# Optimization experiments

Hardware: AMD Instinct MI355X
Metric: run time of the kernel (lower is better)

Reference implementation:

```python
import jax, jax.numpy as jnp
import numpy as np

FP8_MAX = 448.0  # finfo(float8_e4m3fn).max
BLK = 128        # block_size = [128, 128]


def _quant_dequant_act(x):
    """Dynamic per-token, per-128-block fp8 quantization followed by dequant.
    Matches fp8_act_quant: scale = amax(block)/448, q = fp8(x/scale), deq = q*scale."""
    T, K = x.shape
    xb = x.reshape(T, K // BLK, BLK)
    amax = jnp.max(jnp.abs(xb), axis=-1, keepdims=True)
    scale = jnp.maximum(amax, 1e-12) / FP8_MAX  # [T, K//BLK, 1]
    q = (xb / scale).astype(jnp.float8_e4m3fn).astype(jnp.float32)
    return (q * scale).reshape(T, K)


def _dequant_weight(w, s):
    """Block-wise dequant of an fp8-valued [N, K] weight with [N//BLK, K//BLK] scales."""
    N, K = w.shape
    wb = w.reshape(N // BLK, BLK, K // BLK, BLK)
    return (wb * s[:, None, :, None]).reshape(N, K)


def setup_inputs() -> dict:
    key = jax.random.key(0)
    ks = jax.random.split(key, 7)
    T, H, I, E, TOPK = 8192, 2048, 1024, 32, 8
    f8 = lambda x: x.astype(jnp.float8_e4m3fn).astype(jnp.float32)  # store fp8-valued weights as f32
    hidden_states = jax.random.normal(ks[0], (T, H), jnp.float32)
    gate_up_proj = f8(jax.random.normal(ks[1], (E, 2 * I, H), jnp.float32))
    gate_up_proj_scale_inv = jax.random.uniform(ks[2], (E, (2 * I) // BLK, H // BLK), jnp.float32, 0.005, 0.02)
    down_proj = f8(jax.random.normal(ks[3], (E, H, I), jnp.float32))
    down_proj_scale_inv = jax.random.uniform(ks[4], (E, H // BLK, I // BLK), jnp.float32, 0.005, 0.02)
    top_k_index = jax.random.randint(ks[5], (T, TOPK), 0, E, jnp.int32)
    tw = jax.random.uniform(ks[6], (T, TOPK), jnp.float32)
    top_k_weights = tw / jnp.sum(tw, axis=-1, keepdims=True)
    return {
        'hidden_states': hidden_states,
        'gate_up_proj': gate_up_proj,
        'gate_up_proj_scale_inv': gate_up_proj_scale_inv,
        'down_proj': down_proj,
        'down_proj_scale_inv': down_proj_scale_inv,
        'top_k_weights': top_k_weights,
        'top_k_index': top_k_index,
    }


def reference(hidden_states, gate_up_proj, gate_up_proj_scale_inv, down_proj,
              down_proj_scale_inv, top_k_weights, top_k_index):
    E = gate_up_proj.shape[0]
    # Dynamic activation quantization is per-token (expert-independent): do it once.
    x_deq = _quant_dequant_act(hidden_states)  # [T, H]
    # Per-expert combine weight: cw[e, t] = sum_k top_k_weights[t,k] * (top_k_index[t,k]==e)
    hit = top_k_index[None, :, :] == jnp.arange(E, dtype=top_k_index.dtype)[:, None, None]
    cw = jnp.sum(jnp.where(hit, top_k_weights[None, :, :], 0.0), axis=-1)  # [E, T]

    def body(acc, xs):
        wgu, sgu, wd, sd, w_tok = xs
        h = x_deq @ _dequant_weight(wgu, sgu).T          # [T, 2I] fp8 grouped GEMM
        gate, up = jnp.split(h, 2, axis=-1)
        h = jax.nn.silu(gate) * up                        # _apply_gate
        h = _quant_dequant_act(h)                         # re-quantize before down_proj
        y = h @ _dequant_weight(wd, sd).T                 # [T, H]
        return acc + w_tok[:, None] * y, None

    acc0 = jnp.zeros_like(hidden_states, dtype=jnp.float32)
    out, _ = jax.lax.scan(
        body, acc0,
        (gate_up_proj, gate_up_proj_scale_inv, down_proj, down_proj_scale_inv, cw))
    return out
```

## Files before the change

### kernel.cpp

```cpp
#include <hip/hip_runtime.h>

typedef float f32x4 __attribute__((ext_vector_type(4)));
typedef float f32x16 __attribute__((ext_vector_type(16)));
typedef _Float16 f16x4 __attribute__((ext_vector_type(4)));
typedef long long i64t;

constexpr int T = 8192, H = 2048, II = 1024, E = 32, TOPK = 8;
constexpr int NSLOT = T * TOPK;
constexpr int NSLOT_P = NSLOT + E * 16 + 128;
constexpr int MT_MAX = 32;
constexpr int MT1 = 64;

__device__ __forceinline__ void gload16(const unsigned char* g, unsigned char* l) {
  __builtin_amdgcn_global_load_lds((const __attribute__((address_space(1))) unsigned int*)g,
                                   (__attribute__((address_space(3))) unsigned int*)l, 16, 0, 0);
}

__device__ __forceinline__ i64t frag8(const unsigned char* lds, int row, int kbyte) {
  int c8 = (kbyte >> 3) ^ ((row & 7) << 1) ^ ((row >> 3) & 1);
  return *(const i64t*)(lds + row * 128 + c8 * 8);
}
__device__ __forceinline__ void wr16c(unsigned char* lds, int r, int c, uint4 v) {
  if ((r >> 3) & 1) v = make_uint4(v.z, v.w, v.x, v.y);
  *(uint4*)(lds + r * 128 + ((c ^ (r & 7)) << 4)) = v;
}

__global__ void k_quant_x(const float* __restrict__ x, unsigned char* __restrict__ x8,
                          float* __restrict__ xs) {
  int gw = blockIdx.x * 4 + (threadIdx.x >> 6);
  int lane = threadIdx.x & 63;
  int token = gw >> 4, kb = gw & 15;
  float2 v = *(const float2*)(x + (size_t)token * H + kb * 128 + lane * 2);
  float am = fmaxf(fabsf(v.x), fabsf(v.y));
#pragma unroll
  for (int m = 1; m <= 32; m <<= 1) am = fmaxf(am, __shfl_xor(am, m, 64));
  float scale = fmaxf(am, 1e-12f) / 448.0f;
  int pk = __builtin_amdgcn_cvt_pk_fp8_f32(v.x / scale, v.y / scale, 0, false);
  *(unsigned short*)(x8 + (size_t)token * H + kb * 128 + lane * 2) = (unsigned short)(pk & 0xffff);
  if (lane == 0) xs[token * 16 + kb] = scale;
}

__global__ void k_cvt_w_sw(const float* __restrict__ w, unsigned char* __restrict__ w8,
                           int cpr , int nchunk) {
  int i = blockIdx.x * 256 + threadIdx.x;
  if (i >= nchunk) return;
  int row = i / cpr;
  int within = i - row * cpr;
  int kb = within >> 3, pc = within & 7;
  int lc = pc ^ (row & 7);
  int sw = ((row >> 3) & 1) ? 8 : 0;
  const float* src = w + (size_t)row * ((size_t)cpr * 16) + kb * 128 + lc * 16;
  unsigned int o[4];
#pragma unroll
  for (int k = 0; k < 4; ++k) {
    int e0 = (4 * k + sw) & 15;
    f32x4 v = *(const f32x4*)(src + e0);
    int p = __builtin_amdgcn_cvt_pk_fp8_f32(v[0], v[1], 0, false);
    p = __builtin_amdgcn_cvt_pk_fp8_f32(v[2], v[3], p, true);
    o[k] = (unsigned int)p;
  }
  *(uint4*)(w8 + (size_t)i * 16) = make_uint4(o[0], o[1], o[2], o[3]);
}

__global__ void k_count(const int* __restrict__ tki, int* __restrict__ counts) {
  int i = blockIdx.x * 256 + threadIdx.x;
  if (i < NSLOT) atomicAdd(&counts[tki[i]], 1);
}
__global__ void k_scan(const int* __restrict__ counts, int* __restrict__ offsets) {
  if (threadIdx.x == 0) {
    int s = 0;
    for (int e = 0; e < E; ++e) { offsets[e] = s; s += ((counts[e] + 15) >> 4) << 4; }
    offsets[E] = s;
  }
}
__global__ void k_fill(const int* __restrict__ tki, const float* __restrict__ tkw,
                       const int* __restrict__ offsets, int* __restrict__ cursor,
                       int* __restrict__ tok_list, float* __restrict__ cw_list,
                       int* __restrict__ islot) {
  int i = blockIdx.x * 256 + threadIdx.x;
  if (i < NSLOT) {
    int e = tki[i];
    int pos = atomicAdd(&cursor[e], 1);
    int slot = offsets[e] + pos;
    tok_list[slot] = i >> 3;
    cw_list[slot] = tkw[i];
    islot[i] = slot;
  }
}

__launch_bounds__(256, 2)
__global__ void k_gemm1(const unsigned char* __restrict__ x8, const float* __restrict__ xs,
                        const unsigned char* __restrict__ wgu8, const float* __restrict__ sgu,
                        const int* __restrict__ offsets, const int* __restrict__ counts,
                        const int* __restrict__ tok_list,
                        unsigned char* __restrict__ a8, float* __restrict__ ascale) {
  __shared__ __align__(16) unsigned char lA[64 * 128];
  __shared__ __align__(16) unsigned char lBg[2][128 * 128];
  __shared__ __align__(16) unsigned char lBu[2][128 * 128];
  __shared__ float lsx[16 * 64];
  __shared__ int ltok[64];
  __shared__ float lamax[64 * 2];
  __shared__ float lscale[64];

  int bx = blockIdx.x;
  int e = bx >> 9, mt = (bx >> 3) & 63, nt = bx & 7;
  int off0 = offsets[e];
  int Me = counts[e];
  if (mt * 64 >= Me) return;
  int vrows = Me - mt * 64; if (vrows > 64) vrows = 64;
  int tid = threadIdx.x;

  if (tid < 64) ltok[tid] = (tid < vrows) ? tok_list[off0 + mt * 64 + tid] : -1;
  __syncthreads();

  if (tid < 128) {
    int r = tid >> 1, h = tid & 1;
    int tokr = ltok[r]; int tk = tokr < 0 ? 0 : tokr;
#pragma unroll
    for (int i = 0; i < 2; ++i) {
      f32x4 v = *(const f32x4*)(xs + (size_t)tk * 16 + h * 8 + i * 4);
#pragma unroll
      for (int j = 0; j < 4; ++j) lsx[(h * 8 + i * 4 + j) * 64 + r] = (tokr < 0) ? 0.0f : v[j];
    }
  }

  const int lane = tid & 63, wid = tid >> 6;
  const int wm = wid >> 1, wn = wid & 1;
  const int l31 = lane & 31, lg = lane >> 5;

  const int ra = tid >> 2, qa = tid & 3;
  int tokA = ltok[ra] < 0 ? 0 : ltok[ra];
  const unsigned char* gA = x8 + (size_t)tokA * H + qa * 32;

  const int lr = lane >> 3, lc8 = lane & 7;
  const unsigned char* pG[4];
  const unsigned char* pU[4];
#pragma unroll
  for (int i = 0; i < 4; ++i) {
    int row = wid * 32 + i * 8 + lr;
    pG[i] = wgu8 + ((size_t)e * 2048 + nt * 128 + row) * H + lc8 * 16;
    pU[i] = pG[i] + (size_t)1024 * H;
  }

  {
    uint4 a0 = *(const uint4*)gA, a1 = *(const uint4*)(gA + 16);
    wr16c(lA, ra, qa * 2 + 0, a0); wr16c(lA, ra, qa * 2 + 1, a1);
  }
#pragma unroll
  for (int i = 0; i < 4; ++i) {
    gload16(pG[i], lBg[0] + wid * 4096 + i * 1024);
    gload16(pU[i], lBu[0] + wid * 4096 + i * 1024);
  }
  __syncthreads();

  f32x16 aG[2] = {};
  f32x16 aU[2] = {};
  int cur = 0;

  for (int kb = 0; kb < 16; ++kb) {
    uint4 pA0, pA1;
    if (kb < 15) {
#pragma unroll
      for (int i = 0; i < 4; ++i) {
        gload16(pG[i] + (kb + 1) * 128, lBg[cur ^ 1] + wid * 4096 + i * 1024);
        gload16(pU[i] + (kb + 1) * 128, lBu[cur ^ 1] + wid * 4096 + i * 1024);
      }
      pA0 = *(const uint4*)(gA + (kb + 1) * 128);
      pA1 = *(const uint4*)(gA + (kb + 1) * 128 + 16);
    }

    float swg = sgu[(e * 16 + nt) * 16 + kb];
    float swu = sgu[(e * 16 + 8 + nt) * 16 + kb];

    i64t af[8];
#pragma unroll
    for (int ks = 0; ks < 8; ++ks)
      af[ks] = frag8(lA, wm * 32 + l31, ks * 16 + lg * 8);
    f32x4 sxv[4];
#pragma unroll
    for (int jj = 0; jj < 4; ++jj)
      sxv[jj] = *(const f32x4*)(&lsx[kb * 64 + wm * 32 + jj * 8 + lg * 4]);

#pragma unroll
    for (int gu = 0; gu < 2; ++gu) {
      const unsigned char* lB = gu ? lBu[cur] : lBg[cur];
      float sw = gu ? swu : swg;
#pragma unroll
      for (int nf = 0; nf < 2; ++nf) {
        i64t bf[8];
#pragma unroll
        for (int ks = 0; ks < 8; ++ks)
          bf[ks] = frag8(lB, wn * 64 + nf * 32 + l31, ks * 16 + lg * 8);
        f32x16 t = {};
#pragma unroll
        for (int ks = 0; ks < 8; ++ks)
          t = __builtin_amdgcn_mfma_f32_32x32x16_fp8_fp8(af[ks], bf[ks], t, 0, 0, 0);
#pragma unroll
        for (int j = 0; j < 16; ++j) {
          float f = sxv[j >> 2][j & 3] * sw;
          if (gu) aU[nf][j] += t[j] * f; else aG[nf][j] += t[j] * f;
        }
      }
    }

    if (kb < 15) {
      __syncthreads();
      wr16c(lA, ra, qa * 2 + 0, pA0); wr16c(lA, ra, qa * 2 + 1, pA1);
      __syncthreads();
      cur ^= 1;
    }
  }

#pragma unroll
  for (int nf = 0; nf < 2; ++nf)
#pragma unroll
    for (int j = 0; j < 16; ++j) {
      float g = aG[nf][j], u = aU[nf][j];
      aG[nf][j] = g * (1.0f / (1.0f + expf(-g))) * u;
    }

#pragma unroll
  for (int j = 0; j < 16; ++j) {
    float m = fmaxf(fabsf(aG[0][j]), fabsf(aG[1][j]));
#pragma unroll
    for (int msk = 1; msk <= 16; msk <<= 1) m = fmaxf(m, __shfl_xor(m, msk, 64));
    if (l31 == 0)
      lamax[(wm * 32 + (j & 3) + ((j >> 2) * 8) + lg * 4) * 2 + wn] = m;
  }
  __syncthreads();
  if (tid < 64) {
    float mm = fmaxf(lamax[tid * 2], lamax[tid * 2 + 1]);
    lscale[tid] = fmaxf(mm, 1e-12f) / 448.0f;
  }
  __syncthreads();

#pragma unroll
  for (int j = 0; j < 16; ++j) {
    int row = wm * 32 + (j & 3) + ((j >> 2) * 8) + lg * 4;
    float sc = lscale[row];
    int hs = ((row >> 3) & 1) ? 8 : 0;
#pragma unroll
    for (int nf = 0; nf < 2; ++nf) {
      int col = wn * 64 + nf * 32 + l31;
      int pk = __builtin_amdgcn_cvt_pk_fp8_f32(aG[nf][j] / sc, 0.0f, 0, false);
      lA[row * 128 + (((col >> 4) ^ (row & 7)) << 4) + ((col & 15) ^ hs)] = (unsigned char)(pk & 0xff);
    }
    if (row < vrows && l31 == 0 && wn == 0)
      ascale[(off0 + mt * 64 + row) * 8 + nt] = sc;
  }
  __syncthreads();
#pragma unroll
  for (int it = 0; it < 2; ++it) {
    int idx = it * 256 + tid;
    int row = idx >> 3, c = idx & 7;
    if (row < vrows)
      *(uint4*)(a8 + (size_t)(off0 + mt * 64 + row) * 1024 + nt * 128 + c * 16) =
          *(const uint4*)(lA + row * 128 + c * 16);
  }
}

__launch_bounds__(256, 2)
__global__ void k_gemm2(const unsigned char* __restrict__ a8, const float* __restrict__ ascale,
                        const unsigned char* __restrict__ wd8, const float* __restrict__ sd,
                        const int* __restrict__ offsets, const int* __restrict__ counts,
                        const float* __restrict__ cw_list,
                        int ntbase, _Float16* __restrict__ yslot) {
  __shared__ __align__(16) unsigned char lbuf[2][2][128 * 128];
  __shared__ float las[8 * 128];
  __shared__ float lcw[128];

  int bx = blockIdx.x;
  int e = bx >> 8, mt = (bx >> 3) & 31, nth = bx & 7;
  int nt = ntbase + nth;
  int off0 = offsets[e];
  int Me = counts[e];
  if (mt * 128 >= Me) return;
  int vrows = Me - mt * 128; if (vrows > 128) vrows = 128;
  int tid = threadIdx.x;
  const int rowbase = off0 + mt * 128;

  if (tid < 128) lcw[tid] = (tid < vrows) ? cw_list[rowbase + tid] : 0.0f;
  {
    int r = tid >> 1, h = tid & 1;
    int srow = rowbase + r; if (srow > NSLOT_P - 1) srow = NSLOT_P - 1;
    f32x4 v = *(const f32x4*)(ascale + (size_t)srow * 8 + h * 4);
#pragma unroll
    for (int j = 0; j < 4; ++j) las[(h * 4 + j) * 128 + r] = v[j];
  }

  const int lane = tid & 63, wid = tid >> 6;
  const int wm = wid >> 1, wn = wid & 1;
  const int l31 = lane & 31, lg = lane >> 5;

  const int lr = lane >> 3, lc8 = lane & 7;
  const unsigned char* pA[4];
  const unsigned char* pB[4];
#pragma unroll
  for (int i = 0; i < 4; ++i) {
    int row = wid * 32 + i * 8 + lr;
    pA[i] = a8 + (size_t)(rowbase + row) * 1024 + lc8 * 16;
    pB[i] = wd8 + ((size_t)e * 2048 + nt * 128 + row) * 1024 + lc8 * 16;
  }

#pragma unroll
  for (int i = 0; i < 4; ++i) {
    gload16(pA[i], lbuf[0][0] + wid * 4096 + i * 1024);
    gload16(pB[i], lbuf[0][1] + wid * 4096 + i * 1024);
  }
  __syncthreads();

  f32x16 acc[2][2] = {};
  int cur = 0;

  for (int kb = 0; kb < 8; ++kb) {
    if (kb < 7) {
#pragma unroll
      for (int i = 0; i < 4; ++i) {
        gload16(pA[i] + (kb + 1) * 128, lbuf[cur ^ 1][0] + wid * 4096 + i * 1024);
        gload16(pB[i] + (kb + 1) * 128, lbuf[cur ^ 1][1] + wid * 4096 + i * 1024);
      }
    }
    const unsigned char* cA = lbuf[cur][0];
    const unsigned char* cB = lbuf[cur][1];
    float swd = sd[(e * 16 + nt) * 8 + kb];
    i64t bf[2][8];
#pragma unroll
    for (int nf = 0; nf < 2; ++nf)
#pragma unroll
      for (int ks = 0; ks < 8; ++ks)
        bf[nf][ks] = frag8(cB, wn * 64 + nf * 32 + l31, ks * 16 + lg * 8);
#pragma unroll
    for (int mf = 0; mf < 2; ++mf) {
      i64t af[8];
#pragma unroll
      for (int ks = 0; ks < 8; ++ks)
        af[ks] = frag8(cA, wm * 64 + mf * 32 + l31, ks * 16 + lg * 8);
      f32x4 sav[4];
#pragma unroll
      for (int jj = 0; jj < 4; ++jj)
        sav[jj] = *(const f32x4*)(&las[kb * 128 + wm * 64 + mf * 32 + jj * 8 + lg * 4]);
#pragma unroll
      for (int nf = 0; nf < 2; ++nf) {
        f32x16 t = {};
#pragma unroll
        for (int ks = 0; ks < 8; ++ks)
          t = __builtin_amdgcn_mfma_f32_32x32x16_fp8_fp8(af[ks], bf[nf][ks], t, 0, 0, 0);
#pragma unroll
        for (int j = 0; j < 16; ++j)
          acc[mf][nf][j] += t[j] * (sav[j >> 2][j & 3] * swd);
      }
    }
    __syncthreads();
    cur ^= 1;
  }

  _Float16* lh = (_Float16*)lbuf;
#pragma unroll
  for (int mf = 0; mf < 2; ++mf)
#pragma unroll
    for (int j = 0; j < 16; ++j) {
      int row = wm * 64 + mf * 32 + (j & 3) + ((j >> 2) * 8) + lg * 4;
      float w = lcw[row];
#pragma unroll
      for (int nf = 0; nf < 2; ++nf)
        lh[row * 128 + wn * 64 + nf * 32 + l31] = (_Float16)(acc[mf][nf][j] * w);
    }
  __syncthreads();
#pragma unroll
  for (int it = 0; it < 8; ++it) {
    int idx = it * 256 + tid;
    int row = idx >> 4, u = idx & 15;
    if (row < vrows)
      *(uint4*)((char*)yslot + ((size_t)(rowbase + row) * 1024 + nth * 128) * 2 + u * 16) =
          *(const uint4*)((const char*)lh + row * 256 + u * 16);
  }
}

__global__ void k_reduce(const _Float16* __restrict__ yslot, const int* __restrict__ islot,
                         float* __restrict__ out, int half) {
  __shared__ int ls[8];
  int t = blockIdx.x;
  if (threadIdx.x < 8) ls[threadIdx.x] = islot[t * 8 + threadIdx.x];
  __syncthreads();
  int c = threadIdx.x * 4;
  float s0 = 0, s1 = 0, s2 = 0, s3 = 0;
#pragma unroll
  for (int k = 0; k < 8; ++k) {
    f16x4 v = *(const f16x4*)(yslot + (size_t)ls[k] * 1024 + c);
    s0 += (float)v[0]; s1 += (float)v[1]; s2 += (float)v[2]; s3 += (float)v[3];
  }
  f32x4 r = {s0, s1, s2, s3};
  *(f32x4*)(out + (size_t)t * 2048 + half * 1024 + c) = r;
}

extern "C" void kernel_launch(void* const* d_in, const int* in_sizes, int n_in,
                              void* d_out, int out_size, void* d_ws, size_t ws_size,
                              hipStream_t stream) {
  const float* x   = (const float*)d_in[0];
  const float* wgu = (const float*)d_in[1];
  const float* sgu = (const float*)d_in[2];
  const float* wd  = (const float*)d_in[3];
  const float* sd  = (const float*)d_in[4];
  const float* tkw = (const float*)d_in[5];
  const int*   tki = (const int*)d_in[6];
  float* out = (float*)d_out;

  char* ws = (char*)d_ws;
  size_t o = 0;
  auto alloc = [&](size_t sz) { void* p = ws + o; o = (o + sz + 255) & ~(size_t)255; return p; };
  size_t wgu_sz = (size_t)E * 2 * II * H;
  size_t ysl_sz = (size_t)NSLOT_P * II * 2;
  unsigned char* x8    = (unsigned char*)alloc((size_t)T * H);
  unsigned char* wgu8  = (unsigned char*)alloc(wgu_sz > ysl_sz ? wgu_sz : ysl_sz);
  unsigned char* wd8   = (unsigned char*)alloc((size_t)E * H * II);
  unsigned char* a8    = (unsigned char*)alloc((size_t)NSLOT_P * II);
  float* xs            = (float*)alloc((size_t)T * 16 * 4);
  float* as_           = (float*)alloc((size_t)NSLOT_P * 8 * 4);
  int* counts          = (int*)alloc(128);
  int* cursor          = (int*)alloc(128);
  int* offsets         = (int*)alloc(256);
  int* tok_list        = (int*)alloc((size_t)NSLOT_P * 4);
  float* cw_list       = (float*)alloc((size_t)NSLOT_P * 4);
  int* islot           = (int*)alloc((size_t)NSLOT * 4);
  _Float16* yslot      = (_Float16*)wgu8;

  hipMemsetAsync(counts, 0, 128, stream);
  hipMemsetAsync(cursor, 0, 128, stream);

  k_quant_x<<<dim3((T * 16) / 4), dim3(256), 0, stream>>>(x, x8, xs);
  k_cvt_w_sw<<<dim3((E * 2 * II * H / 16) / 256), dim3(256), 0, stream>>>(wgu, wgu8, H / 16, E * 2 * II * H / 16);
  k_cvt_w_sw<<<dim3((E * H * II / 16) / 256), dim3(256), 0, stream>>>(wd, wd8, II / 16, E * H * II / 16);
  k_count<<<dim3(NSLOT / 256), dim3(256), 0, stream>>>(tki, counts);
  k_scan<<<dim3(1), dim3(64), 0, stream>>>(counts, offsets);
  k_fill<<<dim3(NSLOT / 256), dim3(256), 0, stream>>>(tki, tkw, offsets, cursor, tok_list, cw_list, islot);
  k_gemm1<<<dim3(E * MT1 * 8), dim3(256), 0, stream>>>(x8, xs, wgu8, sgu, offsets, counts, tok_list, a8, as_);
  k_gemm2<<<dim3(E * MT_MAX * 8), dim3(256), 0, stream>>>(a8, as_, wd8, sd, offsets, counts, cw_list, 0, yslot);
  k_reduce<<<dim3(T), dim3(256), 0, stream>>>(yslot, islot, out, 0);
  k_gemm2<<<dim3(E * MT_MAX * 8), dim3(256), 0, stream>>>(a8, as_, wd8, sd, offsets, counts, cw_list, 8, yslot);
  k_reduce<<<dim3(T), dim3(256), 0, stream>>>(yslot, islot, out, 1);
}
```

Before: 1.569 ms.

## Drop LDS double buffering in both GEMMs to fit three blocks per CU

Both fp8 grouped GEMM kernels switch from double-buffered LDS tiles with next-k prefetch to a single buffer. Each k-step now loads, synchronises, then computes. This roughly halves LDS per block, and the launch bounds are raised from two to three blocks per CU so more resident blocks can hide memory latency in place of software prefetch. The cost is that loads no longer overlap compute within a block, there is an extra barrier per k-step, and the tighter register budget may force spills.

```diff
diff --git a/kernel.cpp b/kernel.cpp
--- a/kernel.cpp
+++ b/kernel.cpp
@@ -88,15 +88,15 @@
   }
 }
 
-__launch_bounds__(256, 2)
+__launch_bounds__(256, 3)
 __global__ void k_gemm1(const unsigned char* __restrict__ x8, const float* __restrict__ xs,
                         const unsigned char* __restrict__ wgu8, const float* __restrict__ sgu,
                         const int* __restrict__ offsets, const int* __restrict__ counts,
                         const int* __restrict__ tok_list,
                         unsigned char* __restrict__ a8, float* __restrict__ ascale) {
   __shared__ __align__(16) unsigned char lA[64 * 128];
-  __shared__ __align__(16) unsigned char lBg[2][128 * 128];
-  __shared__ __align__(16) unsigned char lBu[2][128 * 128];
+  __shared__ __align__(16) unsigned char lBg[128 * 128];
+  __shared__ __align__(16) unsigned char lBu[128 * 128];
   __shared__ float lsx[16 * 64];
   __shared__ int ltok[64];
   __shared__ float lamax[64 * 2];
@@ -142,32 +142,21 @@
     pU[i] = pG[i] + (size_t)1024 * H;
   }
 
-  {
-    uint4 a0 = *(const uint4*)gA, a1 = *(const uint4*)(gA + 16);
-    wr16c(lA, ra, qa * 2 + 0, a0); wr16c(lA, ra, qa * 2 + 1, a1);
-  }
-#pragma unroll
-  for (int i = 0; i < 4; ++i) {
-    gload16(pG[i], lBg[0] + wid * 4096 + i * 1024);
-    gload16(pU[i], lBu[0] + wid * 4096 + i * 1024);
-  }
-  __syncthreads();
-
   f32x16 aG[2] = {};
   f32x16 aU[2] = {};
-  int cur = 0;
 
   for (int kb = 0; kb < 16; ++kb) {
-    uint4 pA0, pA1;
-    if (kb < 15) {
-#pragma unroll
-      for (int i = 0; i < 4; ++i) {
-        gload16(pG[i] + (kb + 1) * 128, lBg[cur ^ 1] + wid * 4096 + i * 1024);
-        gload16(pU[i] + (kb + 1) * 128, lBu[cur ^ 1] + wid * 4096 + i * 1024);
-      }
-      pA0 = *(const uint4*)(gA + (kb + 1) * 128);
-      pA1 = *(const uint4*)(gA + (kb + 1) * 128 + 16);
-    }
+    uint4 va0 = *(const uint4*)(gA + kb * 128);
+    uint4 va1 = *(const uint4*)(gA + kb * 128 + 16);
+    __syncthreads();
+#pragma unroll
+    for (int i = 0; i < 4; ++i) {
+      gload16(pG[i] + kb * 128, lBg + wid * 4096 + i * 1024);
+      gload16(pU[i] + kb * 128, lBu + wid * 4096 + i * 1024);
+    }
+    wr16c(lA, ra, qa * 2 + 0, va0);
+    wr16c(lA, ra, qa * 2 + 1, va1);
+    __syncthreads();
 
     float swg = sgu[(e * 16 + nt) * 16 + kb];
     float swu = sgu[(e * 16 + 8 + nt) * 16 + kb];
@@ -183,7 +172,7 @@
 
 #pragma unroll
     for (int gu = 0; gu < 2; ++gu) {
-      const unsigned char* lB = gu ? lBu[cur] : lBg[cur];
+      const unsigned char* lB = gu ? lBu : lBg;
       float sw = gu ? swu : swg;
 #pragma unroll
       for (int nf = 0; nf < 2; ++nf) {
@@ -201,13 +190,6 @@
           if (gu) aU[nf][j] += t[j] * f; else aG[nf][j] += t[j] * f;
         }
       }
-    }
-
-    if (kb < 15) {
-      __syncthreads();
-      wr16c(lA, ra, qa * 2 + 0, pA0); wr16c(lA, ra, qa * 2 + 1, pA1);
-      __syncthreads();
-      cur ^= 1;
     }
   }
 
@@ -259,13 +241,13 @@
   }
 }
 
-__launch_bounds__(256, 2)
+__launch_bounds__(256, 3)
 __global__ void k_gemm2(const unsigned char* __restrict__ a8, const float* __restrict__ ascale,
                         const unsigned char* __restrict__ wd8, const float* __restrict__ sd,
                         const int* __restrict__ offsets, const int* __restrict__ counts,
                         const float* __restrict__ cw_list,
                         int ntbase, _Float16* __restrict__ yslot) {
-  __shared__ __align__(16) unsigned char lbuf[2][2][128 * 128];
+  __shared__ __align__(16) unsigned char lbuf[2][128 * 128];
   __shared__ float las[8 * 128];
   __shared__ float lcw[128];
 
@@ -302,26 +284,19 @@
     pB[i] = wd8 + ((size_t)e * 2048 + nt * 128 + row) * 1024 + lc8 * 16;
   }
 
-#pragma unroll
-  for (int i = 0; i < 4; ++i) {
-    gload16(pA[i], lbuf[0][0] + wid * 4096 + i * 1024);
-    gload16(pB[i], lbuf[0][1] + wid * 4096 + i * 1024);
-  }
-  __syncthreads();
-
   f32x16 acc[2][2] = {};
-  int cur = 0;
 
   for (int kb = 0; kb < 8; ++kb) {
-    if (kb < 7) {
-#pragma unroll
-      for (int i = 0; i < 4; ++i) {
-        gload16(pA[i] + (kb + 1) * 128, lbuf[cur ^ 1][0] + wid * 4096 + i * 1024);
-        gload16(pB[i] + (kb + 1) * 128, lbuf[cur ^ 1][1] + wid * 4096 + i * 1024);
-      }
-    }
-    const unsigned char* cA = lbuf[cur][0];
-    const unsigned char* cB = lbuf[cur][1];
+    __syncthreads();
+#pragma unroll
+    for (int i = 0; i < 4; ++i) {
+      gload16(pA[i] + kb * 128, lbuf[0] + wid * 4096 + i * 1024);
+      gload16(pB[i] + kb * 128, lbuf[1] + wid * 4096 + i * 1024);
+    }
+    __syncthreads();
+
+    const unsigned char* cA = lbuf[0];
+    const unsigned char* cB = lbuf[1];
     float swd = sd[(e * 16 + nt) * 8 + kb];
     i64t bf[2][8];
 #pragma unroll
@@ -350,10 +325,9 @@
           acc[mf][nf][j] += t[j] * (sav[j >> 2][j & 3] * swd);
       }
     }
-    __syncthreads();
-    cur ^= 1;
-  }
-
+  }
+
+  __syncthreads();
   _Float16* lh = (_Float16*)lbuf;
 #pragma unroll
   for (int mf = 0; mf < 2; ++mf)
```

Result: slower. 3.318 ms (+111.4%).
